# Optimization experiments

Measured on AMD Instinct MI355X. Metric: run time of the kernel, lower is better.

## Reference

```python
import jax, jax.numpy as jnp
import numpy as np

N, C0, C1 = 8192, 64, 32
P0 = C0 * (C0 + 1) // 2        # 2080 symmetric 0e x 0e pairs
P1 = C1 * (C1 + 1) // 2        # 528 symmetric 1o x 1o pairs -> 0e and 2e
A1 = C1 * (C1 - 1) // 2        # 496 antisymmetric 1o x 1o pairs -> 1e
M0 = C0 + P0 + P1              # 2672 invariant (0e) multiplicities after concat
M1 = C1 + C0 * C1              # 2080 1o multiplicities after concat
NUM_IRREPS = M0 + M1 + A1 + P1 # 5776 total irrep channels (gates)
OUT0, OUT1, OUT1E, OUT2 = 64, 32, 16, 16


def _basis2e():
    # 5 orthonormal (Frobenius) symmetric traceless 3x3 basis matrices: l=2 projection
    s2 = 1.0 / np.sqrt(2.0); s6 = 1.0 / np.sqrt(6.0)
    B = np.zeros((5, 3, 3), np.float32)
    B[0, 0, 1] = B[0, 1, 0] = s2          # xy
    B[1, 1, 2] = B[1, 2, 1] = s2          # yz
    B[2, 0, 2] = B[2, 2, 0] = s2          # xz
    B[3, 0, 0] = s2; B[3, 1, 1] = -s2     # x^2 - y^2
    B[4, 0, 0] = B[4, 1, 1] = -s6; B[4, 2, 2] = 2 * s6  # 2z^2 - x^2 - y^2
    return B


def setup_inputs() -> dict:
    key = jax.random.key(0)
    ks = jax.random.split(key, 8)
    def w(k, shape, fan_in):
        return jax.random.normal(k, shape, jnp.float32) / np.sqrt(fan_in)
    return {
        'x_s': jax.random.normal(ks[0], (N, C0), jnp.float32),
        'x_v': jax.random.normal(ks[1], (N, C1, 3), jnp.float32),
        'mlp_w1': w(ks[2], (M0, M0), M0),
        'mlp_w2': w(ks[3], (M0, NUM_IRREPS), M0),
        'w0': w(ks[4], (M0, OUT0), M0),
        'w1o': w(ks[5], (M1, OUT1), M1),
        'w1e': w(ks[6], (A1, OUT1E), A1),
        'w2e': w(ks[7], (P1, OUT2), P1),
    }


def _forward(x_s, x_v, mlp_w1, mlp_w2, w0, w1o, w1e, w2e):
    n = x_s.shape[0]
    iu0a, iu0b = np.triu_indices(C0)
    c0 = np.where(iu0a == iu0b, 1.0 / np.sqrt(2.0), 1.0).astype(np.float32)
    iu1a, iu1b = np.triu_indices(C1)
    c1 = np.where(iu1a == iu1b, 1.0 / np.sqrt(2.0), 1.0).astype(np.float32)
    ila, ilb = np.triu_indices(C1, k=1)
    B = jnp.asarray(_basis2e())
    # --- tensor square (Clebsch-Gordan contractions) ---
    # 0e x 0e -> 0e (symmetric pairs)
    ss = x_s[:, iu0a] * x_s[:, iu0b] * c0                                   # [n, P0]
    # 1o x 1o symmetric pairs -> 0e (dot) and 2e (sym traceless)
    va, vb = x_v[:, iu1a], x_v[:, iu1b]                                      # [n, P1, 3]
    vv0 = jnp.sum(va * vb, axis=-1) * (c1 / np.sqrt(3.0))                    # [n, P1]
    vv2 = jnp.einsum('npi,npj,kij->npk', va, vb, B) * c1[None, :, None]      # [n, P1, 5]
    # 1o x 1o antisymmetric pairs -> 1e (cross product)
    vv1e = jnp.cross(x_v[:, ila], x_v[:, ilb]) / np.sqrt(2.0)                # [n, A1, 3]
    # 0e x 1o -> 1o
    sv = (x_s[:, :, None, None] * x_v[:, None, :, :]).reshape(n, C0 * C1, 3) # [n, C0*C1, 3]
    # --- concatenate with original features, grouped by irrep ---
    f0 = jnp.concatenate([x_s, ss, vv0], axis=-1)   # [n, M0] invariants
    f1 = jnp.concatenate([x_v, sv], axis=1)         # [n, M1, 3]
    # --- gating MLP on invariants -> one gate per irrep channel ---
    g = jax.nn.silu(f0 @ mlp_w1) @ mlp_w2           # [n, NUM_IRREPS]
    g0 = g[:, :M0]
    g1 = g[:, M0:M0 + M1]
    g1e = g[:, M0 + M1:M0 + M1 + A1]
    g2 = g[:, M0 + M1 + A1:]
    f0 = f0 * g0
    f1 = f1 * g1[:, :, None]
    f1e = vv1e * g1e[:, :, None]
    f2 = vv2 * g2[:, :, None]
    # --- equivariant linear to output irreps (per-l channel mixing) ---
    o0 = f0 @ w0                                    # [n, OUT0]
    o1 = jnp.einsum('nci,co->noi', f1, w1o)         # [n, OUT1, 3]
    o1e = jnp.einsum('nci,co->noi', f1e, w1e)       # [n, OUT1E, 3]
    o2 = jnp.einsum('ncm,co->nom', f2, w2e)         # [n, OUT2, 5]
    return jnp.concatenate([o0, o1.reshape(n, -1), o1e.reshape(n, -1), o2.reshape(n, -1)], axis=-1)


def reference(x_s, x_v, mlp_w1, mlp_w2, w0, w1o, w1e, w2e):
    return _forward(x_s, x_v, mlp_w1, mlp_w2, w0, w1o, w1e, w2e)
```

## Files before the change

### kernel.cpp

```cpp
#include <hip/hip_runtime.h>
#include <hip/hip_bf16.h>
#include <stdint.h>

#define N_ROWS 8192
#define M0C 2672
#define M1C 2080
#define A1C 496
#define P1C 528
#define KP  2688
#define NP2 5888
#define NIR 5776
#define M1P 2112
#define NPAD1 2816

typedef __attribute__((ext_vector_type(8))) _Float16 half8;
typedef __attribute__((ext_vector_type(4))) float floatx4;

__device__ __forceinline__ void async_copy16(const _Float16* g, _Float16* l) {
  __builtin_amdgcn_global_load_lds(
      (__attribute__((address_space(1))) void*)(g),
      (__attribute__((address_space(3))) void*)(l), 16, 0, 0);
}

__global__ __launch_bounds__(256) void transpose_cvt_kernel(
    const float* __restrict__ src, _Float16* __restrict__ dst,
    int srcR, int srcC, int dstC) {
  __shared__ float tile[32][33];
  const int t = threadIdx.x, tx = t & 31, ty = t >> 5;
  const int bx = blockIdx.x, by = blockIdx.y;
#pragma unroll
  for (int i = 0; i < 4; ++i) {
    int sr = bx * 32 + ty + i * 8;
    int sc = by * 32 + tx;
    tile[ty + i * 8][tx] = (sr < srcR && sc < srcC) ? src[(size_t)sr * srcC + sc] : 0.f;
  }
  __syncthreads();
#pragma unroll
  for (int i = 0; i < 4; ++i) {
    int dr = by * 32 + ty + i * 8;
    int dc = bx * 32 + tx;
    dst[(size_t)dr * dstC + dc] = (_Float16)tile[tx][ty + i * 8];
  }
}

__device__ __forceinline__ void triu_ab(int p, int C, int& a, int& b) {
  float fC = (float)C + 0.5f;
  int ai = (int)(fC - sqrtf(fC * fC - 2.0f * (float)p));
  if (ai < 0) ai = 0;
  while (ai > 0 && ai * C - ai * (ai - 1) / 2 > p) --ai;
  while ((ai + 1) * C - (ai + 1) * ai / 2 <= p) ++ai;
  a = ai;
  b = p - (ai * C - ai * (ai - 1) / 2) + ai;
}

__global__ __launch_bounds__(256) void build_f0_kernel(
    const float* __restrict__ xs_g, const float* __restrict__ xv_g,
    _Float16* __restrict__ f0p) {
  __shared__ float xs[64];
  __shared__ float xv[96];
  const int t = threadIdx.x;
  const size_t n = blockIdx.x;
  if (t < 64) xs[t] = xs_g[n * 64 + t];
  else if (t < 160) xv[t - 64] = xv_g[n * 96 + (t - 64)];
  __syncthreads();
  for (int c = t; c < KP; c += 256) {
    float v;
    if (c < 64) {
      v = xs[c];
    } else if (c < 2144) {
      int a, b;
      triu_ab(c - 64, 64, a, b);
      v = xs[a] * xs[b] * ((a == b) ? 0.70710678118654752f : 1.f);
    } else if (c < M0C) {
      int a, b;
      triu_ab(c - 2144, 32, a, b);
      float d = xv[a * 3] * xv[b * 3] + xv[a * 3 + 1] * xv[b * 3 + 1] +
                xv[a * 3 + 2] * xv[b * 3 + 2];
      v = d * ((a == b) ? 0.70710678118654752f : 1.f) * 0.57735026918962576f;
    } else {
      v = 0.f;
    }
    f0p[n * KP + c] = (_Float16)v;
  }
}

template <bool SILU>
__global__ __launch_bounds__(512, 2) void gemm256_kernel(
    const _Float16* __restrict__ A, const _Float16* __restrict__ B,
    _Float16* __restrict__ C, int K, int lda, int ldb, int ldc) {
  __shared__ alignas(16) _Float16 As[4 * 256 * 32];
  __shared__ alignas(16) _Float16 Bs[4 * 256 * 32];
  const int tid = threadIdx.x;

  const int ncol = gridDim.x;
  const int id = blockIdx.y * ncol + blockIdx.x;
  const int xcd = id & 7;
  const int j = id >> 3;
  const int hb = j / (2 * ncol);
  const int w = j - hb * 2 * ncol;
  const int by = xcd * 4 + hb * 2 + (w & 1);
  const int bx = w >> 1;
  const size_t row0 = (size_t)by * 256;
  const size_t col0 = (size_t)bx * 256;

  const _Float16 *pA0, *pA1, *pB0, *pB1;
  _Float16 *lA0, *lA1, *lB0, *lB1;
  {
    int c0 = tid, c1 = tid + 512;
    int r0 = c0 >> 2, ch0 = c0 & 3;
    int r1 = c1 >> 2, ch1 = c1 & 3;
    int s0 = ch0 ^ ((r0 >> 1) & 3);
    int s1 = ch1 ^ ((r1 >> 1) & 3);
    pA0 = A + (row0 + r0) * lda + s0 * 8;
    pA1 = A + (row0 + r1) * lda + s1 * 8;
    pB0 = B + (col0 + r0) * ldb + s0 * 8;
    pB1 = B + (col0 + r1) * ldb + s1 * 8;
    lA0 = &As[c0 * 8]; lA1 = &As[c1 * 8];
    lB0 = &Bs[c0 * 8]; lB1 = &Bs[c1 * 8];
  }

  const int lane = tid & 63;
  const int wv = tid >> 6;
  const int wm = wv & 1;
  const int wn = wv >> 1;
  const int m16 = lane & 15;
  const int quad = lane >> 4;
  const int sw8 = (quad ^ ((m16 >> 1) & 3)) * 8;
  const int aoff = (wm * 128 + m16) * 32 + sw8;
  const int boff = (wn * 64 + m16) * 32 + sw8;

  floatx4 acc[8][4] = {};

#define STAGE(BB)                                             \
  {                                                           \
    async_copy16(pA0, lA0 + (BB) * 8192);                     \
    async_copy16(pA1, lA1 + (BB) * 8192);                     \
    async_copy16(pB0, lB0 + (BB) * 8192);                     \
    async_copy16(pB1, lB1 + (BB) * 8192);                     \
    pA0 += 32; pA1 += 32; pB0 += 32; pB1 += 32;               \
  }

#define KITER(BB, CAA, CBF, CAB, NAA, NBF, VMLIT, DO_STAGE, DO_READN)         \
  {                                                                           \
    if (DO_STAGE) STAGE(((BB) + 3) & 3);                                      \
    asm volatile("s_waitcnt vmcnt(" VMLIT ")" ::: "memory");                  \
    __builtin_amdgcn_s_barrier();                                             \
    __builtin_amdgcn_sched_barrier(0);                                        \
    _Pragma("unroll")                                                         \
    for (int ii = 0; ii < 4; ++ii)                                            \
      CAB[ii] = *(const half8*)&As[(BB) * 8192 + aoff + (ii + 4) * 512];      \
    if (DO_READN) {                                                           \
      _Pragma("unroll")                                                       \
      for (int jj = 0; jj < 4; ++jj)                                          \
        NBF[jj] = *(const half8*)&Bs[(((BB) + 1) & 3) * 8192 + boff + jj * 512]; \
      _Pragma("unroll")                                                       \
      for (int ii = 0; ii < 4; ++ii)                                          \
        NAA[ii] = *(const half8*)&As[(((BB) + 1) & 3) * 8192 + aoff + ii * 512]; \
    }                                                                         \
    __builtin_amdgcn_sched_barrier(0);                                        \
    __builtin_amdgcn_s_setprio(1);                                            \
    _Pragma("unroll")                                                         \
    for (int ii = 0; ii < 4; ++ii)                                            \
      _Pragma("unroll")                                                       \
      for (int jj = 0; jj < 4; ++jj)                                          \
        acc[ii][jj] = __builtin_amdgcn_mfma_f32_16x16x32_f16(                 \
            CAA[ii], CBF[jj], acc[ii][jj], 0, 0, 0);                          \
    __builtin_amdgcn_s_setprio(0);                                            \
    __builtin_amdgcn_sched_barrier(0);                                        \
    __builtin_amdgcn_s_setprio(1);                                            \
    _Pragma("unroll")                                                         \
    for (int ii = 0; ii < 4; ++ii)                                            \
      _Pragma("unroll")                                                       \
      for (int jj = 0; jj < 4; ++jj)                                          \
        acc[ii + 4][jj] = __builtin_amdgcn_mfma_f32_16x16x32_f16(             \
            CAB[ii], CBF[jj], acc[ii + 4][jj], 0, 0, 0);                      \
    __builtin_amdgcn_s_setprio(0);                                            \
    asm volatile("s_waitcnt lgkmcnt(0)" ::: "memory");                        \
  }

  STAGE(0);
  STAGE(1);
  STAGE(2);
  asm volatile("s_waitcnt vmcnt(8)" ::: "memory");
  __builtin_amdgcn_s_barrier();
  __builtin_amdgcn_sched_barrier(0);
  half8 aA0[4], bF0[4], aB0[4], aA1[4], bF1[4], aB1[4];
#pragma unroll
  for (int jj = 0; jj < 4; ++jj) bF0[jj] = *(const half8*)&Bs[boff + jj * 512];
#pragma unroll
  for (int ii = 0; ii < 4; ++ii) aA0[ii] = *(const half8*)&As[aoff + ii * 512];

  const int T = K >> 5;
  for (int t4 = 0; t4 < T - 4; t4 += 4) {
    KITER(0, aA0, bF0, aB0, aA1, bF1, "8", 1, 1);
    KITER(1, aA1, bF1, aB1, aA0, bF0, "8", 1, 1);
    KITER(2, aA0, bF0, aB0, aA1, bF1, "8", 1, 1);
    KITER(3, aA1, bF1, aB1, aA0, bF0, "8", 1, 1);
  }
  KITER(0, aA0, bF0, aB0, aA1, bF1, "8", 1, 1);
  KITER(1, aA1, bF1, aB1, aA0, bF0, "4", 0, 1);
  KITER(2, aA0, bF0, aB0, aA1, bF1, "0", 0, 1);
  KITER(3, aA1, bF1, aB1, aA0, bF0, "0", 0, 0);
#undef KITER
#undef STAGE

#pragma unroll
  for (int ii = 0; ii < 8; ++ii) {
    size_t r = row0 + wm * 128 + ii * 16 + quad * 4;
#pragma unroll
    for (int jj = 0; jj < 4; ++jj) {
      size_t cc = col0 + wn * 64 + jj * 16 + m16;
#pragma unroll
      for (int rr = 0; rr < 4; ++rr) {
        float v = acc[ii][jj][rr];
        if (SILU) v = v / (1.f + __expf(-v));
        C[(r + rr) * ldc + cc] = (_Float16)v;
      }
    }
  }
}

__global__ __launch_bounds__(256) void epi0_kernel(
    const _Float16* __restrict__ f0p, const _Float16* __restrict__ G,
    const _Float16* __restrict__ w0T, float* __restrict__ out) {
  __shared__ alignas(16) _Float16 As[32 * 64];
  const int t = threadIdx.x;
  const size_t n0 = (size_t)blockIdx.x * 32;
  const int lane = t & 63, wave = t >> 6;
  const int m16 = lane & 15, quad = lane >> 4;
  const int rt = (wave & 1) * 16;
  const int ctb = (wave >> 1) * 32;
  const int br = t >> 3, p = t & 7;
  const int l8 = (p ^ (br & 7)) * 8;

  floatx4 acc[2] = {};
  for (int k0 = 0; k0 < KP; k0 += 64) {
    if (k0) __syncthreads();
    {
      half8 f = *(const half8*)&f0p[(n0 + br) * KP + k0 + l8];
      half8 g = *(const half8*)&G[(n0 + br) * NP2 + k0 + l8];
      half8 a;
#pragma unroll
      for (int j = 0; j < 8; ++j) a[j] = (_Float16)((float)f[j] * (float)g[j]);
      *(half8*)&As[br * 64 + p * 8] = a;
    }
    __syncthreads();
#pragma unroll
    for (int kk = 0; kk < 2; ++kk) {
      int q = kk * 4 + quad;
      half8 af = *(const half8*)&As[(rt + m16) * 64 + (q ^ (m16 & 7)) * 8];
#pragma unroll
      for (int c = 0; c < 2; ++c) {
        half8 bf = *(const half8*)&w0T[(size_t)(ctb + c * 16 + m16) * KP + k0 + kk * 32 + quad * 8];
        acc[c] = __builtin_amdgcn_mfma_f32_16x16x32_f16(af, bf, acc[c], 0, 0, 0);
      }
    }
  }
#pragma unroll
  for (int c = 0; c < 2; ++c)
#pragma unroll
    for (int rr = 0; rr < 4; ++rr)
      out[(n0 + rt + quad * 4 + rr) * 288 + ctb + c * 16 + m16] = acc[c][rr];
}

__global__ __launch_bounds__(256) void epi1_kernel(
    const float* __restrict__ xs_g, const float* __restrict__ xv_g,
    const _Float16* __restrict__ G, const _Float16* __restrict__ w1oT,
    float* __restrict__ out) {
  __shared__ float xs[32][64];
  __shared__ float xv[32][96];
  __shared__ alignas(16) _Float16 As[3][32 * 64];
  const int t = threadIdx.x;
  const size_t n0 = (size_t)blockIdx.x * 32;
  for (int idx = t; idx < 32 * 64; idx += 256)
    xs[idx >> 6][idx & 63] = xs_g[(n0 + (idx >> 6)) * 64 + (idx & 63)];
  for (int idx = t; idx < 32 * 96; idx += 256)
    xv[idx / 96][idx % 96] = xv_g[(n0 + idx / 96) * 96 + idx % 96];
  const int lane = t & 63, wave = t >> 6;
  const int m16 = lane & 15, quad = lane >> 4;
  const int rt = (wave & 1) * 16;
  const int ct = (wave >> 1) * 16;
  const int br = t >> 3, p = t & 7;
  const int l8 = (p ^ (br & 7)) * 8;

  floatx4 acc[3] = {};
  __syncthreads();
  for (int k0 = 0; k0 < M1P; k0 += 64) {
    if (k0) __syncthreads();
    {
      half8 g8 = *(const half8*)&G[(n0 + br) * NP2 + M0C + k0 + l8];
      int kbase = k0 + l8;
      half8 a0, a1, a2;
      if (kbase < 32) {
#pragma unroll
        for (int j = 0; j < 8; ++j) {
          float g = (float)g8[j];
          int v = kbase + j;
          a0[j] = (_Float16)(xv[br][v * 3 + 0] * g);
          a1[j] = (_Float16)(xv[br][v * 3 + 1] * g);
          a2[j] = (_Float16)(xv[br][v * 3 + 2] * g);
        }
      } else {
        int s = (kbase - 32) >> 5;
        if (s > 63) s = 63;
        int v0 = (kbase - 32) & 31;
        float xsr = xs[br][s];
#pragma unroll
        for (int j = 0; j < 8; ++j) {
          float g = (float)g8[j] * xsr;
          int v = v0 + j;
          a0[j] = (_Float16)(xv[br][v * 3 + 0] * g);
          a1[j] = (_Float16)(xv[br][v * 3 + 1] * g);
          a2[j] = (_Float16)(xv[br][v * 3 + 2] * g);
        }
      }
      *(half8*)&As[0][br * 64 + p * 8] = a0;
      *(half8*)&As[1][br * 64 + p * 8] = a1;
      *(half8*)&As[2][br * 64 + p * 8] = a2;
    }
    __syncthreads();
#pragma unroll
    for (int kk = 0; kk < 2; ++kk) {
      int q = kk * 4 + quad;
      half8 bf = *(const half8*)&w1oT[(size_t)(ct + m16) * M1P + k0 + kk * 32 + quad * 8];
#pragma unroll
      for (int i = 0; i < 3; ++i) {
        half8 af = *(const half8*)&As[i][(rt + m16) * 64 + (q ^ (m16 & 7)) * 8];
        acc[i] = __builtin_amdgcn_mfma_f32_16x16x32_f16(af, bf, acc[i], 0, 0, 0);
      }
    }
  }
#pragma unroll
  for (int i = 0; i < 3; ++i)
#pragma unroll
    for (int rr = 0; rr < 4; ++rr)
      out[(n0 + rt + quad * 4 + rr) * 288 + 64 + (ct + m16) * 3 + i] = acc[i][rr];
}

__global__ __launch_bounds__(256) void epi1e2_kernel(
    const float* __restrict__ xv_g, const _Float16* __restrict__ G,
    const _Float16* __restrict__ w1eT, const _Float16* __restrict__ w2eT,
    float* __restrict__ out) {
  __shared__ float xv[64][96];
  __shared__ alignas(16) _Float16 As[5][64 * 32];
  __shared__ uint8_t pa[544], pb[544];
  const int t = threadIdx.x;
  const size_t n0 = (size_t)blockIdx.x * 64;
  const int phase = blockIdx.y;
  for (int idx = t; idx < 64 * 96; idx += 256)
    xv[idx / 96][idx % 96] = xv_g[(n0 + idx / 96) * 96 + idx % 96];
  for (int p = t; p < 544; p += 256) {
    int a = 0, b = 0;
    if (phase == 0) {
      if (p < A1C) { triu_ab(p, 31, a, b); b += 1; }
    } else {
      if (p < P1C) triu_ab(p, 32, a, b);
    }
    pa[p] = (uint8_t)a; pb[p] = (uint8_t)b;
  }
  const int lane = t & 63, wave = t >> 6;
  const int m16 = lane & 15, quad = lane >> 4;
  const int sw8 = (quad ^ ((m16 >> 1) & 3)) * 8;
  const int br = t >> 2;
  const int bc8 = ((t & 3) ^ ((br >> 1) & 3)) * 8;
  const int lc8 = (t & 3) * 8;
  const float s2 = 0.70710678118654752f, s6 = 0.40824829046386302f;
  __syncthreads();

  if (phase == 0) {
    floatx4 acc[3] = {};
    for (int k0 = 0; k0 < 512; k0 += 32) {
      if (k0) __syncthreads();
      {
        half8 g8 = *(const half8*)&G[(n0 + br) * NP2 + (M0C + M1C) + k0 + bc8];
        half8 a0, a1, a2;
#pragma unroll
        for (int j = 0; j < 8; ++j) {
          int p = k0 + bc8 + j;
          if (p < A1C) {
            int a = pa[p], b = pb[p];
            float ax = xv[br][a * 3], ay = xv[br][a * 3 + 1], az = xv[br][a * 3 + 2];
            float bx = xv[br][b * 3], by = xv[br][b * 3 + 1], bz = xv[br][b * 3 + 2];
            float g = (float)g8[j] * s2;
            a0[j] = (_Float16)((ay * bz - az * by) * g);
            a1[j] = (_Float16)((az * bx - ax * bz) * g);
            a2[j] = (_Float16)((ax * by - ay * bx) * g);
          } else {
            a0[j] = (_Float16)0.f; a1[j] = (_Float16)0.f; a2[j] = (_Float16)0.f;
          }
        }
        *(half8*)&As[0][br * 32 + lc8] = a0;
        *(half8*)&As[1][br * 32 + lc8] = a1;
        *(half8*)&As[2][br * 32 + lc8] = a2;
      }
      __syncthreads();
      half8 bf = *(const half8*)&w1eT[(size_t)m16 * 512 + k0 + quad * 8];
#pragma unroll
      for (int i = 0; i < 3; ++i) {
        half8 af = *(const half8*)&As[i][(wave * 16 + m16) * 32 + sw8];
        acc[i] = __builtin_amdgcn_mfma_f32_16x16x32_f16(af, bf, acc[i], 0, 0, 0);
      }
    }
#pragma unroll
    for (int i = 0; i < 3; ++i)
#pragma unroll
      for (int rr = 0; rr < 4; ++rr)
        out[(n0 + wave * 16 + quad * 4 + rr) * 288 + 160 + m16 * 3 + i] = acc[i][rr];
  } else {
    floatx4 acc[5] = {};
    for (int k0 = 0; k0 < 544; k0 += 32) {
      if (k0) __syncthreads();
      {
        half8 g8 = *(const half8*)&G[(n0 + br) * NP2 + (M0C + M1C + A1C) + k0 + bc8];
        half8 m0v, m1v, m2v, m3v, m4v;
#pragma unroll
        for (int j = 0; j < 8; ++j) {
          int p = k0 + bc8 + j;
          if (p < P1C) {
            int a = pa[p], b = pb[p];
            float ax = xv[br][a * 3], ay = xv[br][a * 3 + 1], az = xv[br][a * 3 + 2];
            float bx = xv[br][b * 3], by = xv[br][b * 3 + 1], bz = xv[br][b * 3 + 2];
            float c1 = (a == b) ? s2 : 1.f;
            float gw = (float)g8[j] * c1;
            m0v[j] = (_Float16)(s2 * (ax * by + ay * bx) * gw);
            m1v[j] = (_Float16)(s2 * (ay * bz + az * by) * gw);
            m2v[j] = (_Float16)(s2 * (ax * bz + az * bx) * gw);
            m3v[j] = (_Float16)(s2 * (ax * bx - ay * by) * gw);
            m4v[j] = (_Float16)(s6 * (2.f * az * bz - ax * bx - ay * by) * gw);
          } else {
            m0v[j] = (_Float16)0.f; m1v[j] = (_Float16)0.f; m2v[j] = (_Float16)0.f;
            m3v[j] = (_Float16)0.f; m4v[j] = (_Float16)0.f;
          }
        }
        *(half8*)&As[0][br * 32 + lc8] = m0v;
        *(half8*)&As[1][br * 32 + lc8] = m1v;
        *(half8*)&As[2][br * 32 + lc8] = m2v;
        *(half8*)&As[3][br * 32 + lc8] = m3v;
        *(half8*)&As[4][br * 32 + lc8] = m4v;
      }
      __syncthreads();
      half8 bf = *(const half8*)&w2eT[(size_t)m16 * 544 + k0 + quad * 8];
#pragma unroll
      for (int m = 0; m < 5; ++m) {
        half8 af = *(const half8*)&As[m][(wave * 16 + m16) * 32 + sw8];
        acc[m] = __builtin_amdgcn_mfma_f32_16x16x32_f16(af, bf, acc[m], 0, 0, 0);
      }
    }
#pragma unroll
    for (int m = 0; m < 5; ++m)
#pragma unroll
      for (int rr = 0; rr < 4; ++rr)
        out[(n0 + wave * 16 + quad * 4 + rr) * 288 + 208 + m16 * 5 + m] = acc[m][rr];
  }
}

extern "C" void kernel_launch(void* const* d_in, const int* in_sizes, int n_in,
                              void* d_out, int out_size, void* d_ws, size_t ws_size,
                              hipStream_t stream) {
  const float* xs  = (const float*)d_in[0];
  const float* xv  = (const float*)d_in[1];
  const float* w1  = (const float*)d_in[2];
  const float* w2  = (const float*)d_in[3];
  const float* w0  = (const float*)d_in[4];
  const float* w1o = (const float*)d_in[5];
  const float* w1e = (const float*)d_in[6];
  const float* w2e = (const float*)d_in[7];
  float* out = (float*)d_out;

  char* ws = (char*)d_ws;
  size_t off = 0;
  _Float16* w1T = (_Float16*)(ws + off); off += (size_t)NPAD1 * KP * 2;
  _Float16* w2T = (_Float16*)(ws + off); off += (size_t)NP2 * KP * 2;
  _Float16* f0p = (_Float16*)(ws + off); off += (size_t)N_ROWS * KP * 2;
  _Float16* H   = (_Float16*)(ws + off); off += (size_t)N_ROWS * NPAD1 * 2;
  _Float16* G   = (_Float16*)(ws + off);

  _Float16* w0T  = w1T;
  _Float16* w1oT = (_Float16*)((char*)w1T + 344064);
  _Float16* w1eT = (_Float16*)((char*)w1T + 479232);
  _Float16* w2eT = (_Float16*)((char*)w1T + 512000);

  transpose_cvt_kernel<<<dim3(KP / 32, NPAD1 / 32), 256, 0, stream>>>(w1, w1T, M0C, M0C, KP);
  transpose_cvt_kernel<<<dim3(KP / 32, NP2 / 32), 256, 0, stream>>>(w2, w2T, M0C, NIR, KP);
  build_f0_kernel<<<N_ROWS, 256, 0, stream>>>(xs, xv, f0p);
  gemm256_kernel<true><<<dim3(NPAD1 / 256, N_ROWS / 256), 512, 0, stream>>>(
      f0p, w1T, H, KP, KP, KP, NPAD1);
  transpose_cvt_kernel<<<dim3(KP / 32, 2), 256, 0, stream>>>(w0, w0T, M0C, 64, KP);
  transpose_cvt_kernel<<<dim3(M1P / 32, 1), 256, 0, stream>>>(w1o, w1oT, M1C, 32, M1P);
  transpose_cvt_kernel<<<dim3(16, 1), 256, 0, stream>>>(w1e, w1eT, A1C, 16, 512);
  transpose_cvt_kernel<<<dim3(17, 1), 256, 0, stream>>>(w2e, w2eT, P1C, 16, 544);
  gemm256_kernel<false><<<dim3(NP2 / 256, N_ROWS / 256), 512, 0, stream>>>(
      H, w2T, G, KP, NPAD1, KP, NP2);
  epi0_kernel<<<256, 256, 0, stream>>>(f0p, G, w0T, out);
  epi1_kernel<<<256, 256, 0, stream>>>(xs, xv, G, w1oT, out);
  epi1e2_kernel<<<dim3(128, 2), 256, 0, stream>>>(xv, G, w1eT, w2eT, out);
}
```

Measured before the change: 736.2 us.

## Load B fragments directly from global into registers, drop B LDS staging

The GEMM kernel no longer stages the B tile through shared memory. Each wave loads its own B fragments straight from global memory into registers, one k-step ahead, while A keeps its async LDS pipeline with prefetch depth cut from three stages to two. This halves LDS footprint and LDS traffic, which may allow more occupancy and cuts LDS reads. The cost is that B is loaded redundantly by the two wm waves and through uncoalesced per-lane 16-byte loads, with less latency hiding for both operands.

Measured after the change: 819.3 us. 1.11x slower.

```diff
diff --git a/kernel.cpp b/kernel.cpp
--- a/kernel.cpp
+++ b/kernel.cpp
@@ -88,8 +88,7 @@
 __global__ __launch_bounds__(512, 2) void gemm256_kernel(
     const _Float16* __restrict__ A, const _Float16* __restrict__ B,
     _Float16* __restrict__ C, int K, int lda, int ldb, int ldc) {
-  __shared__ alignas(16) _Float16 As[4 * 256 * 32];
-  __shared__ alignas(16) _Float16 Bs[4 * 256 * 32];
+  __shared__ alignas(16) _Float16 As[4 * 8192];
   const int tid = threadIdx.x;
 
   const int ncol = gridDim.x;
@@ -103,8 +102,8 @@
   const size_t row0 = (size_t)by * 256;
   const size_t col0 = (size_t)bx * 256;
 
-  const _Float16 *pA0, *pA1, *pB0, *pB1;
-  _Float16 *lA0, *lA1, *lB0, *lB1;
+  const _Float16 *pA0, *pA1;
+  _Float16 *lA0, *lA1;
   {
     int c0 = tid, c1 = tid + 512;
     int r0 = c0 >> 2, ch0 = c0 & 3;
@@ -113,10 +112,7 @@
     int s1 = ch1 ^ ((r1 >> 1) & 3);
     pA0 = A + (row0 + r0) * lda + s0 * 8;
     pA1 = A + (row0 + r1) * lda + s1 * 8;
-    pB0 = B + (col0 + r0) * ldb + s0 * 8;
-    pB1 = B + (col0 + r1) * ldb + s1 * 8;
     lA0 = &As[c0 * 8]; lA1 = &As[c1 * 8];
-    lB0 = &Bs[c0 * 8]; lB1 = &Bs[c1 * 8];
   }
 
   const int lane = tid & 63;
@@ -127,35 +123,45 @@
   const int quad = lane >> 4;
   const int sw8 = (quad ^ ((m16 >> 1) & 3)) * 8;
   const int aoff = (wm * 128 + m16) * 32 + sw8;
-  const int boff = (wn * 64 + m16) * 32 + sw8;
+
+  const _Float16* pB[4];
+#pragma unroll
+  for (int jj = 0; jj < 4; ++jj)
+    pB[jj] = B + (col0 + wn * 64 + jj * 16 + m16) * (size_t)ldb + quad * 8;
 
   floatx4 acc[8][4] = {};
-
-#define STAGE(BB)                                             \
-  {                                                           \
-    async_copy16(pA0, lA0 + (BB) * 8192);                     \
-    async_copy16(pA1, lA1 + (BB) * 8192);                     \
-    async_copy16(pB0, lB0 + (BB) * 8192);                     \
-    async_copy16(pB1, lB1 + (BB) * 8192);                     \
-    pA0 += 32; pA1 += 32; pB0 += 32; pB1 += 32;               \
-  }
-
-#define KITER(BB, CAA, CBF, CAB, NAA, NBF, VMLIT, DO_STAGE, DO_READN)         \
+  half8 aLo0[4], aLo1[4], aHi[4], bRa[4], bRb[4];
+
+#define STAGE(SLOT)                                   \
+  {                                                   \
+    async_copy16(pA0, lA0 + (SLOT) * 8192);           \
+    async_copy16(pA1, lA1 + (SLOT) * 8192);           \
+    pA0 += 32; pA1 += 32;                             \
+  }
+
+#define BLOAD(BRN)                                    \
+  {                                                   \
+    _Pragma("unroll")                                 \
+    for (int jj = 0; jj < 4; ++jj) {                  \
+      BRN[jj] = *(const half8*)pB[jj];                \
+      pB[jj] += 32;                                   \
+    }                                                 \
+  }
+
+#define KITER(BB, ALOC, ALON, BRC, BRN, VMLIT, DO_STAGE, DO_NEXT)             \
   {                                                                           \
-    if (DO_STAGE) STAGE(((BB) + 3) & 3);                                      \
+    if (DO_STAGE) STAGE(((BB) + 2) & 3);                                      \
+    if (DO_NEXT) BLOAD(BRN);                                                  \
     asm volatile("s_waitcnt vmcnt(" VMLIT ")" ::: "memory");                  \
     __builtin_amdgcn_s_barrier();                                             \
     __builtin_amdgcn_sched_barrier(0);                                        \
     _Pragma("unroll")                                                         \
     for (int ii = 0; ii < 4; ++ii)                                            \
-      CAB[ii] = *(const half8*)&As[(BB) * 8192 + aoff + (ii + 4) * 512];      \
-    if (DO_READN) {                                                           \
-      _Pragma("unroll")                                                       \
-      for (int jj = 0; jj < 4; ++jj)                                          \
-        NBF[jj] = *(const half8*)&Bs[(((BB) + 1) & 3) * 8192 + boff + jj * 512]; \
+      aHi[ii] = *(const half8*)&As[(BB) * 8192 + aoff + (ii + 4) * 512];      \
+    if (DO_NEXT) {                                                            \
       _Pragma("unroll")                                                       \
       for (int ii = 0; ii < 4; ++ii)                                          \
-        NAA[ii] = *(const half8*)&As[(((BB) + 1) & 3) * 8192 + aoff + ii * 512]; \
+        ALON[ii] = *(const half8*)&As[(((BB) + 1) & 3) * 8192 + aoff + ii * 512]; \
     }                                                                         \
     __builtin_amdgcn_sched_barrier(0);                                        \
     __builtin_amdgcn_s_setprio(1);                                            \
@@ -164,7 +170,7 @@
       _Pragma("unroll")                                                       \
       for (int jj = 0; jj < 4; ++jj)                                          \
         acc[ii][jj] = __builtin_amdgcn_mfma_f32_16x16x32_f16(                 \
-            CAA[ii], CBF[jj], acc[ii][jj], 0, 0, 0);                          \
+            ALOC[ii], BRC[jj], acc[ii][jj], 0, 0, 0);                         \
     __builtin_amdgcn_s_setprio(0);                                            \
     __builtin_amdgcn_sched_barrier(0);                                        \
     __builtin_amdgcn_s_setprio(1);                                            \
@@ -173,35 +179,33 @@
       _Pragma("unroll")                                                       \
       for (int jj = 0; jj < 4; ++jj)                                          \
         acc[ii + 4][jj] = __builtin_amdgcn_mfma_f32_16x16x32_f16(             \
-            CAB[ii], CBF[jj], acc[ii + 4][jj], 0, 0, 0);                      \
+            aHi[ii], BRC[jj], acc[ii + 4][jj], 0, 0, 0);                      \
     __builtin_amdgcn_s_setprio(0);                                            \
     asm volatile("s_waitcnt lgkmcnt(0)" ::: "memory");                        \
   }
 
   STAGE(0);
   STAGE(1);
-  STAGE(2);
-  asm volatile("s_waitcnt vmcnt(8)" ::: "memory");
+  BLOAD(bRa);
+  asm volatile("s_waitcnt vmcnt(6)" ::: "memory");
   __builtin_amdgcn_s_barrier();
   __builtin_amdgcn_sched_barrier(0);
-  half8 aA0[4], bF0[4], aB0[4], aA1[4], bF1[4], aB1[4];
-#pragma unroll
-  for (int jj = 0; jj < 4; ++jj) bF0[jj] = *(const half8*)&Bs[boff + jj * 512];
-#pragma unroll
-  for (int ii = 0; ii < 4; ++ii) aA0[ii] = *(const half8*)&As[aoff + ii * 512];
+#pragma unroll
+  for (int ii = 0; ii < 4; ++ii) aLo0[ii] = *(const half8*)&As[aoff + ii * 512];
 
   const int T = K >> 5;
   for (int t4 = 0; t4 < T - 4; t4 += 4) {
-    KITER(0, aA0, bF0, aB0, aA1, bF1, "8", 1, 1);
-    KITER(1, aA1, bF1, aB1, aA0, bF0, "8", 1, 1);
-    KITER(2, aA0, bF0, aB0, aA1, bF1, "8", 1, 1);
-    KITER(3, aA1, bF1, aB1, aA0, bF0, "8", 1, 1);
-  }
-  KITER(0, aA0, bF0, aB0, aA1, bF1, "8", 1, 1);
-  KITER(1, aA1, bF1, aB1, aA0, bF0, "4", 0, 1);
-  KITER(2, aA0, bF0, aB0, aA1, bF1, "0", 0, 1);
-  KITER(3, aA1, bF1, aB1, aA0, bF0, "0", 0, 0);
+    KITER(0, aLo0, aLo1, bRa, bRb, "6", 1, 1);
+    KITER(1, aLo1, aLo0, bRb, bRa, "6", 1, 1);
+    KITER(2, aLo0, aLo1, bRa, bRb, "6", 1, 1);
+    KITER(3, aLo1, aLo0, bRb, bRa, "6", 1, 1);
+  }
+  KITER(0, aLo0, aLo1, bRa, bRb, "6", 1, 1);
+  KITER(1, aLo1, aLo0, bRb, bRa, "6", 1, 1);
+  KITER(2, aLo0, aLo1, bRa, bRb, "4", 0, 1);
+  KITER(3, aLo1, aLo0, bRb, bRa, "0", 0, 0);
 #undef KITER
+#undef BLOAD
 #undef STAGE
 
 #pragma unroll
```
